# Kernel tuning notes

Measured on AMD Instinct MI355X. Metric: run time of the kernel, lower is better.

Reference implementation:

```python
import jax, jax.numpy as jnp
import numpy as np

N, D = 32768, 256  # n_nodes, in_dim == mem_dim


def setup_inputs() -> dict:
    key = jax.random.key(0)
    ks = jax.random.split(key, 8)
    inputs = jax.random.normal(ks[0], (N, D), jnp.float32)
    state = jax.random.normal(ks[1], (1, D), jnp.float32)  # initial root cell state
    s = 1.0 / np.sqrt(D)  # pytorch default uniform init bound
    root_W = jax.random.uniform(ks[2], (D, D), jnp.float32, -s, s)
    root_b = jax.random.uniform(ks[3], (D,), jnp.float32, -s, s)
    W_ih = jax.random.uniform(ks[4], (4 * D, D), jnp.float32, -s, s)
    W_hh = jax.random.uniform(ks[5], (4 * D, D), jnp.float32, -s, s)
    b_ih = jax.random.uniform(ks[6], (4 * D,), jnp.float32, -s, s)
    b_hh = jax.random.uniform(ks[7], (4 * D,), jnp.float32, -s, s)
    # topologically ordered random tree: parents[i] < i, node 0 is root
    rng = np.random.default_rng(0)
    raw = rng.integers(0, N, size=N)
    parents = jnp.asarray(np.minimum(raw, np.maximum(np.arange(N) - 1, 0)).astype(np.int64))
    idx = jnp.arange(N, dtype=jnp.int64)  # node -> input row (tree.idx)
    return dict(inputs=inputs, state=state, root_W=root_W, root_b=root_b,
                W_ih=W_ih, W_hh=W_hh, b_ih=b_ih, b_hh=b_hh,
                parents=parents, idx=idx)


def reference(inputs, state, root_W, root_b, W_ih, W_hh, b_ih, b_hh, parents, idx):
    n, d = inputs.shape
    # root: tanh(Linear(inputs[root_idx])), cell state = given state
    h0 = jnp.tanh(inputs[idx[0]] @ root_W.T + root_b)
    c0 = state[0]
    H = jnp.zeros((n, d), inputs.dtype).at[0].set(h0)
    C = jnp.zeros((n, d), inputs.dtype).at[0].set(c0)

    def step(carry, i):
        H, C = carry
        p = parents[i]
        x = inputs[idx[i]]
        # torch nn.LSTMCell: gates = x W_ih^T + b_ih + h W_hh^T + b_hh
        gates = x @ W_ih.T + b_ih + H[p] @ W_hh.T + b_hh
        ig, fg, gg, og = jnp.split(gates, 4)
        c = jax.nn.sigmoid(fg) * C[p] + jax.nn.sigmoid(ig) * jnp.tanh(gg)
        h = jax.nn.sigmoid(og) * jnp.tanh(c)
        return (H.at[i].set(h), C.at[i].set(c)), None

    (H, C), _ = jax.lax.scan(step, (H, C), jnp.arange(1, n))
    # topdown_hidden_traversal: scatter each node's hidden into a [n_inputs, mem_dim] buffer
    hiddens = jnp.zeros((n, d), inputs.dtype).at[idx].set(H)
    # (root topdown_state, root topdown hidden, all hiddens)
    return C[0:1], H[0:1], hiddens
```

## Files before the change

### kernel.cpp

```cpp
#include <hip/hip_runtime.h>


#define NN 32768
#define DD 256
#define GP 1024
#define SENT_C 0x7FC00001u
#define SENT_H 0xFFFFFFFFu

typedef __attribute__((ext_vector_type(8))) short short8;
typedef __attribute__((ext_vector_type(4))) float float4_;
typedef __attribute__((ext_vector_type(4))) unsigned uint4_;

static __device__ __forceinline__ unsigned short f2bf(float f) {
    unsigned u = __builtin_bit_cast(unsigned, f);
    unsigned r = u + 0x7FFFu + ((u >> 16) & 1u);
    return (unsigned short)(r >> 16);
}
static __device__ __forceinline__ float bf2f(unsigned short u) {
    unsigned v = ((unsigned)u) << 16;
    return __builtin_bit_cast(float, v);
}
static __device__ __forceinline__ float sigf(float x) { return 1.0f / (1.0f + __expf(-x)); }
static __device__ __forceinline__ float tanh_(float x) { return 1.0f - 2.0f / (__expf(2.0f * x) + 1.0f); }

__global__ void k_init(int* cnt, int* cur, int* maxd, float* C, unsigned* HbU) {
    const int g = blockIdx.x * 256 + threadIdx.x;
    if (g < NN + 2) { cnt[g] = 0; cur[g] = 0; }
    if (g == 0) maxd[0] = 0;
    const uint4_ sc = (uint4_){SENT_C, SENT_C, SENT_C, SENT_C};
    const uint4_ sh = (uint4_){SENT_H, SENT_H, SENT_H, SENT_H};
    uint4_* Cu = (uint4_*)C;
    uint4_* Hu = (uint4_*)HbU;
    #pragma unroll
    for (int k = 0; k < 4; ++k) Cu[(size_t)g + (size_t)k * 524288] = sc;
    #pragma unroll
    for (int k = 0; k < 2; ++k) Hu[(size_t)g + (size_t)k * 524288] = sh;
}

__global__ void k_root(const float* __restrict__ X, const float* __restrict__ state,
                       const float* __restrict__ rootW, const float* __restrict__ rootb,
                       const int* __restrict__ idx,
                       unsigned short* __restrict__ Hb, float* __restrict__ C) {
    const int t = threadIdx.x;
    const int row = idx[0];
    const float4_* xr = (const float4_*)(X + (size_t)row * DD);
    const float4_* wr = (const float4_*)(rootW + (size_t)t * DD);
    float acc = rootb[t];
    for (int k = 0; k < DD / 4; ++k) {
        float4_ a = xr[k], b = wr[k];
        acc += a[0] * b[0] + a[1] * b[1] + a[2] * b[2] + a[3] * b[3];
    }
    Hb[t] = f2bf(tanh_(acc));
    C[t] = state[t];
}

__global__ void k_dep_init(const int* __restrict__ parents, int* dep, int* jmp) {
    int i = blockIdx.x * 256 + threadIdx.x;
    if (i >= NN) return;
    dep[i] = (i == 0) ? 0 : 1;
    jmp[i] = (i == 0) ? 0 : parents[i];
}

__global__ void k_dep_step(const int* __restrict__ depA, const int* __restrict__ jmpA,
                           int* __restrict__ depB, int* __restrict__ jmpB) {
    int i = blockIdx.x * 256 + threadIdx.x;
    if (i >= NN) return;
    int j = jmpA[i];
    depB[i] = depA[i] + depA[j];
    jmpB[i] = jmpA[j];
}

__global__ void k_hist(const int* __restrict__ dep, int* cnt, int* maxd) {
    int i = blockIdx.x * 256 + threadIdx.x;
    if (i >= NN) return;
    int d = dep[i];
    atomicAdd(&cnt[d], 1);
    atomicMax(&maxd[0], d);
}

__global__ void k_scan(const int* __restrict__ cnt, int* __restrict__ off) {
    __shared__ int sums[256];
    const int tid = threadIdx.x;
    const int base = tid * 128;
    int s = 0;
    for (int k = 0; k < 128; ++k) s += cnt[base + k];
    sums[tid] = s;
    __syncthreads();
    if (tid == 0) {
        int run = 0;
        for (int t = 0; t < 256; ++t) { int tmp = sums[t]; sums[t] = run; run += tmp; }
    }
    __syncthreads();
    int run = sums[tid];
    for (int k = 0; k < 128; ++k) { off[base + k] = run; run += cnt[base + k]; }
    if (tid == 255) off[NN] = run;
}

__global__ void k_scatter(const int* __restrict__ dep, const int* __restrict__ off,
                          int* cur, int* __restrict__ lev) {
    int i = blockIdx.x * 256 + threadIdx.x;
    if (i >= NN) return;
    int d = dep[i];
    int pos = off[d] + atomicAdd(&cur[d], 1);
    lev[pos] = i;
}

__global__ __launch_bounds__(256, 1) void k_gx(
    const float* __restrict__ X, const float* __restrict__ Wih,
    const float* __restrict__ bih, const float* __restrict__ bhh,
    const int* __restrict__ idx, unsigned short* __restrict__ Gp) {
    __shared__ __align__(16) short bw_s[128 * 264];
    __shared__ float bias_s[128];
    const int tid = threadIdx.x;
    const int w = tid >> 6, l = tid & 63;
    const int lanelo = l & 15, quad = l >> 4;

    short8 a[2][8];
    #pragma unroll
    for (int ti = 0; ti < 2; ++ti) {
        int n = (blockIdx.x * 8 + w * 2 + ti) * 16 + lanelo;
        int row = idx[n];
        const float* xp = X + (size_t)row * DD + quad * 8;
        #pragma unroll
        for (int ks = 0; ks < 8; ++ks) {
            float4_ x0 = *(const float4_*)(xp + ks * 32);
            float4_ x1 = *(const float4_*)(xp + ks * 32 + 4);
            short8 s;
            s[0] = f2bf(x0[0]); s[1] = f2bf(x0[1]); s[2] = f2bf(x0[2]); s[3] = f2bf(x0[3]);
            s[4] = f2bf(x1[0]); s[5] = f2bf(x1[1]); s[6] = f2bf(x1[2]); s[7] = f2bf(x1[3]);
            a[ti][ks] = s;
        }
    }
    for (int gc = 0; gc < 8; ++gc) {
        __syncthreads();
        for (int e = tid; e < 128 * 64; e += 256) {
            int r = e >> 6, c4 = (e & 63) * 4;
            float4_ b = *(const float4_*)(Wih + (size_t)(gc * 128 + r) * DD + c4);
            unsigned short* pb = (unsigned short*)&bw_s[r * 264 + c4];
            pb[0] = f2bf(b[0]); pb[1] = f2bf(b[1]); pb[2] = f2bf(b[2]); pb[3] = f2bf(b[3]);
        }
        if (tid < 128) bias_s[tid] = bih[gc * 128 + tid] + bhh[gc * 128 + tid];
        __syncthreads();
        #pragma unroll
        for (int ntl = 0; ntl < 8; ++ntl) {
            float4_ acc0 = (float4_){0.f, 0.f, 0.f, 0.f};
            float4_ acc1 = (float4_){0.f, 0.f, 0.f, 0.f};
            #pragma unroll
            for (int ks = 0; ks < 8; ++ks) {
                short8 bf = *(const short8*)&bw_s[(ntl * 16 + lanelo) * 264 + ks * 32 + quad * 8];
                acc0 = __builtin_amdgcn_mfma_f32_16x16x32_bf16(a[0][ks], bf, acc0, 0, 0, 0);
                acc1 = __builtin_amdgcn_mfma_f32_16x16x32_bf16(a[1][ks], bf, acc1, 0, 0, 0);
            }
            float bia = bias_s[ntl * 16 + lanelo];
            int g = gc * 128 + ntl * 16 + lanelo;
            int nb0 = (blockIdx.x * 8 + w * 2) * 16 + quad * 4;
            #pragma unroll
            for (int r = 0; r < 4; ++r) {
                Gp[(size_t)(nb0 + r) * GP + g] = f2bf(acc0[r] + bia);
                Gp[(size_t)(nb0 + 16 + r) * GP + g] = f2bf(acc1[r] + bia);
            }
        }
    }
}

__global__ __launch_bounds__(256, 1) void k_tree2(
    const float* __restrict__ Whh,
    const int* __restrict__ parents,
    const int* __restrict__ off, const int* __restrict__ lev, const int* __restrict__ maxd_g,
    const unsigned short* __restrict__ Gp,
    unsigned short* __restrict__ Hb, float* __restrict__ C) {

    __shared__ __align__(16) short w_s[128 * 264];
    __shared__ __align__(16) short A_s[16 * 264];
    __shared__ __align__(16) float G_s[16 * 128];
    __shared__ __align__(16) float R_s[16 * 132];
    __shared__ int nd_s[16], par_s[16];

    const int tid = threadIdx.x;
    const int j = blockIdx.x & 7, grp = blockIdx.x >> 3;
    const int w = tid >> 6, l = tid & 63;
    const int lanelo = l & 15, quad = l >> 4;

    for (int e = tid; e < 128 * 64; e += 256) {
        int r = e >> 6, c4 = (e & 63) * 4;
        int G = ((r >> 5) * 256) + j * 32 + (r & 31);
        float4_ b = *(const float4_*)(Whh + (size_t)G * DD + c4);
        unsigned short* pb = (unsigned short*)&w_s[r * 264 + c4];
        pb[0] = f2bf(b[0]); pb[1] = f2bf(b[1]); pb[2] = f2bf(b[2]); pb[3] = f2bf(b[3]);
    }
    __syncthreads();

    const unsigned* HbU = (const unsigned*)Hb;
    const int maxd = maxd_g[0];
    int lo = off[1];
    for (int d = 1; d <= maxd; ++d) {
        const int hi = off[d + 1];
        const int tiles = (hi - lo + 15) >> 4;
        for (int t = grp; t < tiles; t += 32) {
            const int base = lo + t * 16;
            if (tid < 16) {
                int node = -1, p = 0;
                if (base + tid < hi) { node = lev[base + tid]; p = parents[node]; }
                nd_s[tid] = node; par_s[tid] = p;
            }
            __syncthreads();
            {
                int m = tid >> 4, q8 = (tid & 15) * 8;
                int seg = q8 >> 5, cc = q8 & 31;
                float4_ g01 = (float4_){0.f, 0.f, 0.f, 0.f};
                float4_ g23 = (float4_){0.f, 0.f, 0.f, 0.f};
                if (nd_s[m] >= 0) {
                    const unsigned short* gp =
                        Gp + (size_t)nd_s[m] * GP + seg * 256 + j * 32 + cc;
                    short8 gv = *(const short8*)gp;
                    g01[0] = bf2f(gv[0]); g01[1] = bf2f(gv[1]); g01[2] = bf2f(gv[2]); g01[3] = bf2f(gv[3]);
                    g23[0] = bf2f(gv[4]); g23[1] = bf2f(gv[5]); g23[2] = bf2f(gv[6]); g23[3] = bf2f(gv[7]);
                }
                *(float4_*)&G_s[m * 128 + q8] = g01;
                *(float4_*)&G_s[m * 128 + q8 + 4] = g23;
            }
            if (tid < 64) {
                const int m = tid & 15;
                const bool act = (tid < 16) && (nd_s[m] >= 0);
                const unsigned* sp = &HbU[(size_t)par_s[m] * 128 + j * 16];
                bool miss = act && (__hip_atomic_load(sp, __ATOMIC_RELAXED,
                                                      __HIP_MEMORY_SCOPE_AGENT) == SENT_H);
                while (__any(miss ? 1 : 0))
                    miss = act && (__hip_atomic_load(sp, __ATOMIC_RELAXED,
                                                     __HIP_MEMORY_SCOPE_AGENT) == SENT_H);
            }
            __syncthreads();
            const int m0 = tid >> 5, c0 = tid & 31, col = j * 32 + c0;
            float* cpp0 = &C[(size_t)par_s[m0] * DD + col];
            float* cpp1 = &C[(size_t)par_s[m0 + 8] * DD + col];
            float cp0 = __hip_atomic_load(cpp0, __ATOMIC_RELAXED, __HIP_MEMORY_SCOPE_AGENT);
            float cp1 = __hip_atomic_load(cpp1, __ATOMIC_RELAXED, __HIP_MEMORY_SCOPE_AGENT);
            unsigned hv[8];
            #pragma unroll
            for (int k2 = 0; k2 < 8; ++k2) {
                const int e = tid + k2 * 256, m = e >> 7, cu = e & 127;
                hv[k2] = (nd_s[m] >= 0)
                    ? __hip_atomic_load(&HbU[(size_t)par_s[m] * 128 + cu],
                                        __ATOMIC_RELAXED, __HIP_MEMORY_SCOPE_AGENT)
                    : 0u;
            }
            if (nd_s[m0] >= 0)
                while (__builtin_bit_cast(unsigned, cp0) == SENT_C) {
                    __builtin_amdgcn_s_sleep(1);
                    cp0 = __hip_atomic_load(cpp0, __ATOMIC_RELAXED, __HIP_MEMORY_SCOPE_AGENT);
                }
            if (nd_s[m0 + 8] >= 0)
                while (__builtin_bit_cast(unsigned, cp1) == SENT_C) {
                    __builtin_amdgcn_s_sleep(1);
                    cp1 = __hip_atomic_load(cpp1, __ATOMIC_RELAXED, __HIP_MEMORY_SCOPE_AGENT);
                }
            #pragma unroll
            for (int k2 = 0; k2 < 8; ++k2) {
                const int e = tid + k2 * 256, m = e >> 7, cu = e & 127;
                if (nd_s[m] >= 0)
                    while (hv[k2] == SENT_H) {
                        __builtin_amdgcn_s_sleep(1);
                        hv[k2] = __hip_atomic_load(&HbU[(size_t)par_s[m] * 128 + cu],
                                                   __ATOMIC_RELAXED, __HIP_MEMORY_SCOPE_AGENT);
                    }
            }
            #pragma unroll
            for (int k2 = 0; k2 < 8; ++k2) {
                const int e = tid + k2 * 256, m = e >> 7, cu = e & 127;
                *(unsigned*)&A_s[m * 264 + cu * 2] = hv[k2];
            }
            __syncthreads();
            {
                short8 af[8];
                #pragma unroll
                for (int ks = 0; ks < 8; ++ks)
                    af[ks] = *(const short8*)&A_s[lanelo * 264 + ks * 32 + quad * 8];
                #pragma unroll
                for (int ti = 0; ti < 2; ++ti) {
                    int ntl = w * 2 + ti;
                    float4_ acc = (float4_){0.f, 0.f, 0.f, 0.f};
                    #pragma unroll
                    for (int ks = 0; ks < 8; ++ks) {
                        short8 bf = *(const short8*)&w_s[(ntl * 16 + lanelo) * 264 + ks * 32 + quad * 8];
                        acc = __builtin_amdgcn_mfma_f32_16x16x32_bf16(af[ks], bf, acc, 0, 0, 0);
                    }
                    #pragma unroll
                    for (int r = 0; r < 4; ++r)
                        R_s[(quad * 4 + r) * 132 + ntl * 16 + lanelo] = acc[r];
                }
            }
            __syncthreads();
            {
                #pragma unroll
                for (int pass = 0; pass < 2; ++pass) {
                    int m = m0 + pass * 8;
                    float cp = pass ? cp1 : cp0;
                    float ig = R_s[m * 132 + c0]      + G_s[m * 128 + c0];
                    float fg = R_s[m * 132 + 32 + c0] + G_s[m * 128 + 32 + c0];
                    float gg = R_s[m * 132 + 64 + c0] + G_s[m * 128 + 64 + c0];
                    float og = R_s[m * 132 + 96 + c0] + G_s[m * 128 + 96 + c0];
                    float cn = sigf(fg) * cp + sigf(ig) * tanh_(gg);
                    float hn = sigf(og) * tanh_(cn);
                    int node = nd_s[m];
                    unsigned short hs = f2bf(hn);
                    unsigned pair = ((unsigned)hs) |
                                    (((unsigned)(unsigned short)__shfl_down((int)hs, 1)) << 16);
                    if (node >= 0) {
                        __hip_atomic_store(&C[(size_t)node * DD + col], cn,
                                           __ATOMIC_RELAXED, __HIP_MEMORY_SCOPE_AGENT);
                        if ((c0 & 1) == 0)
                            __hip_atomic_store(&((unsigned*)Hb)[(size_t)node * 128 + (col >> 1)],
                                               pair, __ATOMIC_RELAXED, __HIP_MEMORY_SCOPE_AGENT);
                    }
                }
            }
            __builtin_amdgcn_fence(__ATOMIC_RELEASE, "workgroup");
            __syncthreads();
        }
        lo = hi;
    }
}

__global__ void k_out(const unsigned short* __restrict__ Hb, const float* __restrict__ C,
                      const int* __restrict__ idx, float* __restrict__ out) {
    const int b = blockIdx.x, t = threadIdx.x;
    if (b < NN) {
        int drow = idx[b];
        out[512 + (size_t)drow * DD + t] = bf2f(Hb[(size_t)b * DD + t]);
    } else {
        out[t] = C[t];
        out[DD + t] = bf2f(Hb[t]);
    }
}

extern "C" void kernel_launch(void* const* d_in, const int* in_sizes, int n_in,
                              void* d_out, int out_size, void* d_ws, size_t ws_size,
                              hipStream_t stream) {
    const float* X     = (const float*)d_in[0];
    const float* state = (const float*)d_in[1];
    const float* rootW = (const float*)d_in[2];
    const float* rootb = (const float*)d_in[3];
    const float* Wih   = (const float*)d_in[4];
    const float* Whh   = (const float*)d_in[5];
    const float* bih   = (const float*)d_in[6];
    const float* bhh   = (const float*)d_in[7];
    const int* parents = (const int*)d_in[8];
    const int* idx     = (const int*)d_in[9];

    float* C           = (float*)d_ws;
    unsigned short* Hb = (unsigned short*)(C + (size_t)NN * DD);
    unsigned short* Gp = Hb + (size_t)NN * DD;
    int* ip            = (int*)(Gp + (size_t)NN * GP);
    int* depA = ip;            ip += NN;
    int* jmpA = ip;            ip += NN;
    int* depB = ip;            ip += NN;
    int* jmpB = ip;            ip += NN;
    int* cnt  = ip;            ip += NN + 2;
    int* off  = ip;            ip += NN + 2;
    int* cur  = ip;            ip += NN + 2;
    int* lev  = ip;            ip += NN;
    int* maxd = ip;            ip += 4;
    float* out = (float*)d_out;

    k_init<<<dim3(2048), dim3(256), 0, stream>>>(cnt, cur, maxd, C, (unsigned*)Hb);
    k_root<<<dim3(1), dim3(256), 0, stream>>>(X, state, rootW, rootb, idx, Hb, C);

    k_dep_init<<<dim3(128), dim3(256), 0, stream>>>(parents, depA, jmpA);
    int* dA = depA; int* jA = jmpA; int* dB = depB; int* jB = jmpB;
    for (int it = 0; it < 15; ++it) {
        k_dep_step<<<dim3(128), dim3(256), 0, stream>>>(dA, jA, dB, jB);
        int* tp;
        tp = dA; dA = dB; dB = tp;
        tp = jA; jA = jB; jB = tp;
    }
    k_hist<<<dim3(128), dim3(256), 0, stream>>>(dA, cnt, maxd);
    k_scan<<<dim3(1), dim3(256), 0, stream>>>(cnt, off);
    k_scatter<<<dim3(128), dim3(256), 0, stream>>>(dA, off, cur, lev);

    k_gx<<<dim3(256), dim3(256), 0, stream>>>(X, Wih, bih, bhh, idx, Gp);
    k_tree2<<<dim3(256), dim3(256), 0, stream>>>(Whh, parents, off, lev, maxd, Gp, Hb, C);
    k_out<<<dim3(NN + 1), dim3(256), 0, stream>>>(Hb, C, idx, out);
}
```

Measured before the change: 1.856 ms.

## Add optimistic readiness fast path, prefetch next tile metadata, stage level offsets in LDS

The tree-LSTM level loop now loads parent H and C speculatively and checks every value for sentinels with one block-wide vote. It only falls back to the old poll-and-barrier wait when some value is not ready, which removes a barrier and a polling round from the common path. It also prefetches the next tile's node and parent indices, including those of the next level, into registers during the current tile. Level offsets are staged in shared memory to avoid repeated global loads. This adds LDS use and complexity in the synchronisation logic.

```diff
diff --git a/kernel.cpp b/kernel.cpp
--- a/kernel.cpp
+++ b/kernel.cpp
@@ -4,6 +4,7 @@
 #define NN 32768
 #define DD 256
 #define GP 1024
+#define OFFCAP 4096
 #define SENT_C 0x7FC00001u
 #define SENT_H 0xFFFFFFFFu
 
@@ -174,6 +175,7 @@
     __shared__ __align__(16) short A_s[16 * 264];
     __shared__ __align__(16) float G_s[16 * 128];
     __shared__ __align__(16) float R_s[16 * 132];
+    __shared__ int off_s[OFFCAP];
     __shared__ int nd_s[16], par_s[16];
 
     const int tid = threadIdx.x;
@@ -188,21 +190,33 @@
         unsigned short* pb = (unsigned short*)&w_s[r * 264 + c4];
         pb[0] = f2bf(b[0]); pb[1] = f2bf(b[1]); pb[2] = f2bf(b[2]); pb[3] = f2bf(b[3]);
     }
+    const int maxd = maxd_g[0];
+    const int staged = (maxd + 2 < OFFCAP) ? (maxd + 2) : OFFCAP;
+    for (int e = tid; e < staged; e += 256) off_s[e] = off[e];
     __syncthreads();
 
+    #define OFFS(i) (((i) < staged) ? off_s[(i)] : off[(i)])
+
     const unsigned* HbU = (const unsigned*)Hb;
-    const int maxd = maxd_g[0];
-    int lo = off[1];
+    int pn_node = -1, pn_par = 0;
+    bool pn_valid = false;
+
+    int lo = OFFS(1);
     for (int d = 1; d <= maxd; ++d) {
-        const int hi = off[d + 1];
+        const int hi = OFFS(d + 1);
         const int tiles = (hi - lo + 15) >> 4;
         for (int t = grp; t < tiles; t += 32) {
             const int base = lo + t * 16;
             if (tid < 16) {
-                int node = -1, p = 0;
-                if (base + tid < hi) { node = lev[base + tid]; p = parents[node]; }
-                nd_s[tid] = node; par_s[tid] = p;
-            }
+                if (pn_valid) {
+                    nd_s[tid] = pn_node; par_s[tid] = pn_par;
+                } else {
+                    int node = -1, p = 0;
+                    if (base + tid < hi) { node = lev[base + tid]; p = parents[node]; }
+                    nd_s[tid] = node; par_s[tid] = p;
+                }
+            }
+            pn_valid = false;
             __syncthreads();
             {
                 int m = tid >> 4, q8 = (tid & 15) * 8;
@@ -219,23 +233,31 @@
                 *(float4_*)&G_s[m * 128 + q8] = g01;
                 *(float4_*)&G_s[m * 128 + q8 + 4] = g23;
             }
-            if (tid < 64) {
-                const int m = tid & 15;
-                const bool act = (tid < 16) && (nd_s[m] >= 0);
-                const unsigned* sp = &HbU[(size_t)par_s[m] * 128 + j * 16];
-                bool miss = act && (__hip_atomic_load(sp, __ATOMIC_RELAXED,
-                                                      __HIP_MEMORY_SCOPE_AGENT) == SENT_H);
-                while (__any(miss ? 1 : 0))
-                    miss = act && (__hip_atomic_load(sp, __ATOMIC_RELAXED,
-                                                     __HIP_MEMORY_SCOPE_AGENT) == SENT_H);
-            }
-            __syncthreads();
+            {
+                int nt_base = -1, nt_hi = hi;
+                if (t + 32 < tiles) {
+                    nt_base = lo + (t + 32) * 16;
+                } else if (d < maxd) {
+                    const int hi2 = OFFS(d + 2);
+                    const int tiles2 = (hi2 - hi + 15) >> 4;
+                    if (grp < tiles2) { nt_base = hi + grp * 16; nt_hi = hi2; }
+                }
+                if (nt_base >= 0) {
+                    if (tid < 16) {
+                        int node = -1, p = 0;
+                        if (nt_base + tid < nt_hi) { node = lev[nt_base + tid]; p = parents[node]; }
+                        pn_node = node; pn_par = p;
+                    }
+                    pn_valid = true;
+                }
+            }
             const int m0 = tid >> 5, c0 = tid & 31, col = j * 32 + c0;
             float* cpp0 = &C[(size_t)par_s[m0] * DD + col];
             float* cpp1 = &C[(size_t)par_s[m0 + 8] * DD + col];
             float cp0 = __hip_atomic_load(cpp0, __ATOMIC_RELAXED, __HIP_MEMORY_SCOPE_AGENT);
             float cp1 = __hip_atomic_load(cpp1, __ATOMIC_RELAXED, __HIP_MEMORY_SCOPE_AGENT);
             unsigned hv[8];
+            bool ok = true;
             #pragma unroll
             for (int k2 = 0; k2 < 8; ++k2) {
                 const int e = tid + k2 * 256, m = e >> 7, cu = e & 127;
@@ -243,26 +265,42 @@
                     ? __hip_atomic_load(&HbU[(size_t)par_s[m] * 128 + cu],
                                         __ATOMIC_RELAXED, __HIP_MEMORY_SCOPE_AGENT)
                     : 0u;
-            }
-            if (nd_s[m0] >= 0)
-                while (__builtin_bit_cast(unsigned, cp0) == SENT_C) {
-                    __builtin_amdgcn_s_sleep(1);
-                    cp0 = __hip_atomic_load(cpp0, __ATOMIC_RELAXED, __HIP_MEMORY_SCOPE_AGENT);
-                }
-            if (nd_s[m0 + 8] >= 0)
-                while (__builtin_bit_cast(unsigned, cp1) == SENT_C) {
-                    __builtin_amdgcn_s_sleep(1);
-                    cp1 = __hip_atomic_load(cpp1, __ATOMIC_RELAXED, __HIP_MEMORY_SCOPE_AGENT);
-                }
-            #pragma unroll
-            for (int k2 = 0; k2 < 8; ++k2) {
-                const int e = tid + k2 * 256, m = e >> 7, cu = e & 127;
-                if (nd_s[m] >= 0)
-                    while (hv[k2] == SENT_H) {
+                if (nd_s[m] >= 0 && hv[k2] == SENT_H) ok = false;
+            }
+            if (nd_s[m0] >= 0 && __builtin_bit_cast(unsigned, cp0) == SENT_C) ok = false;
+            if (nd_s[m0 + 8] >= 0 && __builtin_bit_cast(unsigned, cp1) == SENT_C) ok = false;
+            if (!__syncthreads_and(ok ? 1 : 0)) {
+                if (tid < 64) {
+                    const int m = tid & 15;
+                    const bool act = (tid < 16) && (nd_s[m] >= 0);
+                    const unsigned* sp = &HbU[(size_t)par_s[m] * 128 + j * 16];
+                    bool miss = act && (__hip_atomic_load(sp, __ATOMIC_RELAXED,
+                                                          __HIP_MEMORY_SCOPE_AGENT) == SENT_H);
+                    while (__any(miss ? 1 : 0))
+                        miss = act && (__hip_atomic_load(sp, __ATOMIC_RELAXED,
+                                                         __HIP_MEMORY_SCOPE_AGENT) == SENT_H);
+                }
+                __syncthreads();
+                if (nd_s[m0] >= 0)
+                    while (__builtin_bit_cast(unsigned, cp0) == SENT_C) {
                         __builtin_amdgcn_s_sleep(1);
-                        hv[k2] = __hip_atomic_load(&HbU[(size_t)par_s[m] * 128 + cu],
-                                                   __ATOMIC_RELAXED, __HIP_MEMORY_SCOPE_AGENT);
+                        cp0 = __hip_atomic_load(cpp0, __ATOMIC_RELAXED, __HIP_MEMORY_SCOPE_AGENT);
                     }
+                if (nd_s[m0 + 8] >= 0)
+                    while (__builtin_bit_cast(unsigned, cp1) == SENT_C) {
+                        __builtin_amdgcn_s_sleep(1);
+                        cp1 = __hip_atomic_load(cpp1, __ATOMIC_RELAXED, __HIP_MEMORY_SCOPE_AGENT);
+                    }
+                #pragma unroll
+                for (int k2 = 0; k2 < 8; ++k2) {
+                    const int e = tid + k2 * 256, m = e >> 7, cu = e & 127;
+                    if (nd_s[m] >= 0)
+                        while (hv[k2] == SENT_H) {
+                            __builtin_amdgcn_s_sleep(1);
+                            hv[k2] = __hip_atomic_load(&HbU[(size_t)par_s[m] * 128 + cu],
+                                                       __ATOMIC_RELAXED, __HIP_MEMORY_SCOPE_AGENT);
+                        }
+                }
             }
             #pragma unroll
             for (int k2 = 0; k2 < 8; ++k2) {
@@ -319,6 +357,7 @@
         }
         lo = hi;
     }
+    #undef OFFS
 }
 
 __global__ void k_out(const unsigned short* __restrict__ Hb, const float* __restrict__ C,
```

Measured after the change: 1.764 ms. 1.05x faster.
